# Kernel optimization log

Measured on AMD Instinct MI355X. Metric: run time of the kernel, lower is better.

Reference implementation:

```python
import jax, jax.numpy as jnp
import numpy as np

H = 224; W = 224; ZNEAR = 0.01; ZFAR = 100.0; EPS2D = 0.3
N_GAUSS = 1024; N_CAM = 2
ALPHA_MIN = 1.0 / 255.0; ALPHA_MAX = 0.999


def quat_to_rotmat(q):
    # gsplat convention: wxyz, normalized internally. q: [N,4] -> [N,3,3]
    q = q / jnp.linalg.norm(q, axis=-1, keepdims=True)
    w, x, y, z = q[:, 0], q[:, 1], q[:, 2], q[:, 3]
    R = jnp.stack([
        jnp.stack([1.0 - 2.0 * (y * y + z * z), 2.0 * (x * y - w * z), 2.0 * (x * z + w * y)], -1),
        jnp.stack([2.0 * (x * y + w * z), 1.0 - 2.0 * (x * x + z * z), 2.0 * (y * z - w * x)], -1),
        jnp.stack([2.0 * (x * z - w * y), 2.0 * (y * z + w * x), 1.0 - 2.0 * (x * x + y * y)], -1),
    ], -2)
    return R


def setup_inputs() -> dict:
    key = jax.random.key(0)
    ks = jax.random.split(key, 5)
    xyz = jax.random.normal(ks[0], (N_GAUSS, 3), dtype=jnp.float32) * 0.5
    rgb = jax.random.uniform(ks[1], (N_GAUSS, 3), dtype=jnp.float32)
    opacity = jax.random.uniform(ks[2], (N_GAUSS,), dtype=jnp.float32)
    scale = jax.random.uniform(ks[3], (N_GAUSS, 3), dtype=jnp.float32) * 0.04 + 0.005
    rotation = jax.random.normal(ks[4], (N_GAUSS, 4), dtype=jnp.float32)
    w2c_list = []
    for a in (0.0, 0.3):  # two views, small yaw apart, camera 3 units back
        c, s = np.cos(a), np.sin(a)
        w2c_list.append(np.array([[c, 0, -s, 0], [0, 1, 0, 0], [s, 0, c, 3.0], [0, 0, 0, 1]], dtype=np.float32))
    w2cs = jnp.asarray(np.stack(w2c_list))
    K = np.array([[300.0, 0.0, 112.0], [0.0, 300.0, 112.0], [0.0, 0.0, 1.0]], dtype=np.float32)
    Ks = jnp.asarray(np.stack([K] * N_CAM))
    return {"w2cs": w2cs, "Ks": Ks, "xyz": xyz, "rgb": rgb, "opacity": opacity, "scale": scale, "rotation": rotation}


def _render_one(viewmat, K, means, cov3d, colors, opac, bg):
    R = viewmat[:3, :3]; t = viewmat[:3, 3]
    p_cam = means @ R.T + t                       # [N,3]
    z = p_cam[:, 2]; rz = 1.0 / z
    fx, fy, cx, cy = K[0, 0], K[1, 1], K[0, 2], K[1, 2]
    lim_x = 1.3 * (0.5 * W / fx); lim_y = 1.3 * (0.5 * H / fy)
    tx = z * jnp.clip(p_cam[:, 0] * rz, -lim_x, lim_x)
    ty = z * jnp.clip(p_cam[:, 1] * rz, -lim_y, lim_y)
    # camera-frame 3D covariance, then perspective Jacobian projection to 2D
    cov_cam = jnp.einsum('ij,njk,lk->nil', R, cov3d, R)   # [N,3,3]
    zero = jnp.zeros_like(rz)
    J = jnp.stack([
        jnp.stack([fx * rz, zero, -fx * tx * rz * rz], -1),
        jnp.stack([zero, fy * rz, -fy * ty * rz * rz], -1),
    ], -2)                                                # [N,2,3]
    cov2d = jnp.einsum('nij,njk,nlk->nil', J, cov_cam, J) # [N,2,2]
    a = cov2d[:, 0, 0] + EPS2D; d = cov2d[:, 1, 1] + EPS2D; b = cov2d[:, 0, 1]
    det = a * d - b * b
    ia = d / det; id_ = a / det; ib = -b / det            # inverse of blurred 2D cov
    u = fx * p_cam[:, 0] * rz + cx
    v = fy * p_cam[:, 1] * rz + cy
    valid = (z > ZNEAR) & (z < ZFAR) & (det > 0)
    o = jnp.where(valid, opac, 0.0)
    # front-to-back depth sort (gradients flow through gathered values)
    order = jnp.argsort(z)
    u, v, ia, ib, id_, o = (arr[order] for arr in (u, v, ia, ib, id_, o))
    colors_s = colors[order]
    # pixel centers, row-major flattened grid [P]
    xs = jnp.arange(W, dtype=jnp.float32) + 0.5
    ys = jnp.arange(H, dtype=jnp.float32) + 0.5
    pix_x = jnp.tile(xs, H); pix_y = jnp.repeat(ys, W)
    dx = u[None, :] - pix_x[:, None]                      # [P,N]
    dy = v[None, :] - pix_y[:, None]
    sigma = 0.5 * (ia * dx * dx + id_ * dy * dy) + ib * dx * dy
    alpha = jnp.minimum(o[None, :] * jnp.exp(-sigma), ALPHA_MAX)
    alpha = jnp.where((sigma >= 0.0) & (alpha > ALPHA_MIN), alpha, 0.0)
    log1m = jnp.log1p(-alpha)
    logT = jnp.cumsum(log1m, axis=1)
    T = jnp.exp(logT - log1m)                             # exclusive transmittance
    wgt = alpha * T                                       # [P,N]
    img = wgt @ colors_s                                  # [P,3]
    Tf = jnp.exp(logT[:, -1])
    img = img + Tf[:, None] * bg
    return img.reshape(H, W, 3), (1.0 - Tf).reshape(H, W, 1)


def reference(w2cs, Ks, xyz, rgb, opacity, scale, rotation):
    Rq = quat_to_rotmat(rotation)                         # [N,3,3]
    M = Rq * scale[:, None, :]                            # R @ diag(s)
    cov3d = jnp.einsum('nij,nkj->nik', M, M)              # R S S^T R^T
    bg = jnp.ones((3,), dtype=xyz.dtype)                  # bg_color buffer of ones
    imgs, alphas = jax.vmap(lambda vm, K: _render_one(vm, K, xyz, cov3d, rgb, opacity, bg))(w2cs, Ks)
    return imgs, alphas                                   # rgb [C,H,W,3], mask [C,H,W,1]
```

## Files before the change

kernel.cpp:

```cpp
#include <hip/hip_runtime.h>
#include <math.h>

#define NG 1024
#define NC 2
#define HH 224
#define WW 224
#define TILES_X 28
#define TILES_Y 28
#define EPS2D 0.3f
#define ALPHA_MIN (1.0f/255.0f)
#define ALPHA_MAX 0.999f
#define MAXL 512
#define LOG2E 1.4426950408889634f

__global__ __launch_bounds__(256) void fused_kernel(
        const float* __restrict__ w2cs, const float* __restrict__ Ks,
        const float* __restrict__ xyz, const float* __restrict__ rgb,
        const float* __restrict__ opac, const float* __restrict__ scale,
        const float* __restrict__ rot, float* __restrict__ out) {
    const int cam = blockIdx.z;
    const int TX = blockIdx.x, TY = blockIdx.y;
    const int tid = threadIdx.x;
    const int lane = tid & 63;
    const int wv   = tid >> 6;

    __shared__ union {
        unsigned long long keys[MAXL];
        float4 part[4][64];
    } shu;
    __shared__ float4 sA[MAXL];
    __shared__ float4 sB[MAXL];
    __shared__ float  sC[MAXL];
    __shared__ int    cnt[8];
    __shared__ int    scnt;

    if (tid == 0) scnt = 0;
    __syncthreads();

    const float* vm = w2cs + cam*16;
    const float R00 = vm[0],  R01 = vm[1],  R02 = vm[2],  t0 = vm[3];
    const float R10 = vm[4],  R11 = vm[5],  R12 = vm[6],  t1 = vm[7];
    const float R20 = vm[8],  R21 = vm[9],  R22 = vm[10], t2 = vm[11];
    const float* Kc = Ks + cam*9;
    const float fx = Kc[0], cx = Kc[2], fy = Kc[4], cy = Kc[5];
    const float limx = 1.3f * (0.5f * (float)WW / fx);
    const float limy = 1.3f * (0.5f * (float)HH / fy);

    #pragma unroll
    for (int k = 0; k < 4; k++) {
        int g = k*256 + tid;
        float X = xyz[g*3], Y = xyz[g*3+1], Z = xyz[g*3+2];
        float pz = R20*X + R21*Y + R22*Z + t2;
        float o  = opac[g];
        float tau = __logf(255.f * o);
        bool cand = (pz > 0.01f) && (pz < 100.f) && (tau > 0.f);
        if (cand) {
            float rz = 1.f / pz;
            float px = R00*X + R01*Y + R02*Z + t0;
            float py = R10*X + R11*Y + R12*Z + t1;
            float uu = fx*px*rz + cx;
            float vv = fy*py*rz + cy;
            float sx = scale[g*3+0], sy = scale[g*3+1], sz = scale[g*3+2];
            float smax = fmaxf(sx, fmaxf(sy, sz));
            float j00 = fx*rz, j11 = fy*rz;
            float j02m = fx*limx*rz, j12m = fy*limy*rz;
            float abnd = smax*smax*(j00*j00 + j02m*j02m) + EPS2D;
            float dbnd = smax*smax*(j11*j11 + j12m*j12m) + EPS2D;
            float rx = sqrtf(2.f*tau*abnd) + 0.01f;
            float ry = sqrtf(2.f*tau*dbnd) + 0.01f;
            int xmin = max((int)ceilf (uu - rx - 0.5f), 0);
            int xmax = min((int)floorf(uu + rx - 0.5f), WW-1);
            int ymin = max((int)ceilf (vv - ry - 0.5f), 0);
            int ymax = min((int)floorf(vv + ry - 0.5f), HH-1);
            cand = (xmin <= xmax) && (ymin <= ymax) &&
                   (TX >= (xmin>>3)) && (TX <= (xmax>>3)) &&
                   (TY >= (ymin>>3)) && (TY <= (ymax>>3));
        }
        unsigned long long m = __ballot(cand);
        int cw = __popcll(m);
        if (cw) {
            int basepos = 0;
            if (lane == 0) basepos = atomicAdd(&scnt, cw);
            basepos = __shfl(basepos, 0);
            if (cand) {
                int pos = basepos + __popcll(m & ((1ull << lane) - 1ull));
                if (pos < MAXL)
                    shu.keys[pos] = ((unsigned long long)__float_as_uint(pz) << 10)
                                  | (unsigned long long)g;
            }
        }
    }
    __syncthreads();
    int n = min(scnt, MAXL);

    unsigned long long myk0 = (tid       < n) ? shu.keys[tid]       : 0ull;
    unsigned long long myk1 = (tid + 256 < n) ? shu.keys[tid + 256] : 0ull;
    int r0 = 0, r1 = 0;
    #pragma unroll 4
    for (int j = 0; j < n; j++) {
        unsigned long long kj = shu.keys[j];
        r0 += (kj < myk0) ? 1 : 0;
        r1 += (kj < myk1) ? 1 : 0;
    }
    __syncthreads();
    if (tid       < n) shu.keys[r0] = myk0;
    if (tid + 256 < n) shu.keys[r1] = myk1;
    __syncthreads();

    auto prep = [&](int i, float4 &A, float4 &B, float &C) -> bool {
        if (i >= n) return false;
        int g = (int)(shu.keys[i] & 1023ull);

        float qw = rot[g*4+0], qx = rot[g*4+1], qy = rot[g*4+2], qz = rot[g*4+3];
        float qn = rsqrtf(qw*qw + qx*qx + qy*qy + qz*qz);
        qw *= qn; qx *= qn; qy *= qn; qz *= qn;
        float r00 = 1.f - 2.f*(qy*qy + qz*qz), r01 = 2.f*(qx*qy - qw*qz), r02 = 2.f*(qx*qz + qw*qy);
        float r10 = 2.f*(qx*qy + qw*qz), r11 = 1.f - 2.f*(qx*qx + qz*qz), r12 = 2.f*(qy*qz - qw*qx);
        float r20 = 2.f*(qx*qz - qw*qy), r21 = 2.f*(qy*qz + qw*qx), r22 = 1.f - 2.f*(qx*qx + qy*qy);

        float sx = scale[g*3+0], sy = scale[g*3+1], sz = scale[g*3+2];
        float m00 = r00*sx, m01 = r01*sy, m02 = r02*sz;
        float m10 = r10*sx, m11 = r11*sy, m12 = r12*sz;
        float m20 = r20*sx, m21 = r21*sy, m22 = r22*sz;
        float c00 = m00*m00 + m01*m01 + m02*m02;
        float c01 = m00*m10 + m01*m11 + m02*m12;
        float c02 = m00*m20 + m01*m21 + m02*m22;
        float c11 = m10*m10 + m11*m11 + m12*m12;
        float c12 = m10*m20 + m11*m21 + m12*m22;
        float c22 = m20*m20 + m21*m21 + m22*m22;

        float X = xyz[g*3], Y = xyz[g*3+1], Z = xyz[g*3+2];
        float px = R00*X + R01*Y + R02*Z + t0;
        float py = R10*X + R11*Y + R12*Z + t1;
        float pz = R20*X + R21*Y + R22*Z + t2;
        float rz = 1.f / pz;

        float txc = pz * fminf(fmaxf(px*rz, -limx), limx);
        float tyc = pz * fminf(fmaxf(py*rz, -limy), limy);

        float v00 = R00*c00 + R01*c01 + R02*c02;
        float v01 = R00*c01 + R01*c11 + R02*c12;
        float v02 = R00*c02 + R01*c12 + R02*c22;
        float v10 = R10*c00 + R11*c01 + R12*c02;
        float v11 = R10*c01 + R11*c11 + R12*c12;
        float v12 = R10*c02 + R11*c12 + R12*c22;
        float v20 = R20*c00 + R21*c01 + R22*c02;
        float v21 = R20*c01 + R21*c11 + R22*c12;
        float v22 = R20*c02 + R21*c12 + R22*c22;
        float cc00 = v00*R00 + v01*R01 + v02*R02;
        float cc01 = v00*R10 + v01*R11 + v02*R12;
        float cc02 = v00*R20 + v01*R21 + v02*R22;
        float cc11 = v10*R10 + v11*R11 + v12*R12;
        float cc12 = v10*R20 + v11*R21 + v12*R22;
        float cc22 = v20*R20 + v21*R21 + v22*R22;

        float j00 = fx*rz, j02 = -fx*txc*rz*rz;
        float j11 = fy*rz, j12 = -fy*tyc*rz*rz;
        float a  = j00*j00*cc00 + 2.f*j00*j02*cc02 + j02*j02*cc22 + EPS2D;
        float bq = j00*j11*cc01 + j00*j12*cc02 + j02*j11*cc12 + j02*j12*cc22;
        float d  = j11*j11*cc11 + 2.f*j11*j12*cc12 + j12*j12*cc22 + EPS2D;
        float det = a*d - bq*bq;

        if (!((pz > 0.01f) && (pz < 100.f) && (det > 0.f))) return false;

        float o = opac[g];
        float tau = __logf(255.f * o);
        if (!(tau > 0.f)) return false;

        float hx = sqrtf(2.f*tau*a) + 0.02f;
        float hy = sqrtf(2.f*tau*d) + 0.02f;
        float uu = fx*px*rz + cx;
        float vv = fy*py*rz + cy;
        float xlo = (float)(TX*8) + 0.5f, xhi = (float)(TX*8) + 7.5f;
        float ylo = (float)(TY*8) + 0.5f, yhi = (float)(TY*8) + 7.5f;
        if (uu + hx < xlo || uu - hx > xhi || vv + hy < ylo || vv - hy > yhi)
            return false;

        float idet = 1.f / det;
        A = make_float4(uu, vv, 0.5f*LOG2E*d*idet, -LOG2E*bq*idet);
        B = make_float4(0.5f*LOG2E*a*idet, o, rgb[g*3+0], rgb[g*3+1]);
        C = rgb[g*3+2];
        return true;
    };

    float4 A0, B0, A1, B1; float C0, C1;
    bool kp0 = prep(tid,       A0, B0, C0);
    bool kp1 = prep(tid + 256, A1, B1, C1);

    unsigned long long bal0 = __ballot(kp0);
    unsigned long long bal1 = __ballot(kp1);
    if (lane == 0) { cnt[wv] = __popcll(bal0); cnt[4 + wv] = __popcll(bal1); }
    __syncthreads();
    int base0 = 0, base1 = 0, n2 = 0;
    #pragma unroll
    for (int s = 0; s < 8; s++) {
        int cs = cnt[s];
        base0 += (s < wv)     ? cs : 0;
        base1 += (s < 4 + wv) ? cs : 0;
        n2 += cs;
    }
    unsigned long long lt = (1ull << lane) - 1ull;
    int d0 = base0 + __popcll(bal0 & lt);
    int d1 = base1 + __popcll(bal1 & lt);
    if (kp0) { sA[d0] = A0; sB[d0] = B0; sC[d0] = C0; }
    if (kp1) { sA[d1] = A1; sB[d1] = B1; sC[d1] = C1; }
    __syncthreads();

    const float pxl = (float)(TX*8 + (lane & 7)) + 0.5f;
    const float pyl = (float)(TY*8 + (lane >> 3)) + 0.5f;
    int seglen = (n2 + 3) >> 2;
    int js = wv * seglen;
    int je = min(n2, js + seglen);

    float T = 1.f, cr = 0.f, cg = 0.f, cb = 0.f;
#define CBODY(J) do { \
        float4 ga = sA[J]; float4 gb = sB[J]; float bv = sC[J]; \
        float dx = ga.x - pxl, dy = ga.y - pyl; \
        float sg = ga.z*dx*dx + gb.x*dy*dy + ga.w*dx*dy; \
        float al = fminf(gb.y * exp2f(-sg), ALPHA_MAX); \
        al = (sg >= 0.f && al > ALPHA_MIN) ? al : 0.f; \
        float wgt = al * T; \
        cr += wgt * gb.z; cg += wgt * gb.w; cb += wgt * bv; \
        T -= al * T; \
    } while (0)

    int j = js;
    while (j + 16 <= je) {
        #pragma unroll 4
        for (int q = 0; q < 16; q++) { CBODY(j + q); }
        j += 16;
        if (__all(T < 1e-4f)) break;
    }
    for (; j < je; j++) { CBODY(j); }
#undef CBODY

    shu.part[wv][lane] = make_float4(cr, cg, cb, T);
    __syncthreads();

    if (tid < 64) {
        float4 c0 = shu.part[0][lane];
        float Cr = c0.x, Cg = c0.y, Cb = c0.z, Tp = c0.w;
        #pragma unroll
        for (int s = 1; s < 4; s++) {
            float4 cs = shu.part[s][lane];
            Cr += Tp * cs.x;
            Cg += Tp * cs.y;
            Cb += Tp * cs.z;
            Tp *= cs.w;
        }
        int p = (TY*8 + (lane >> 3)) * WW + TX*8 + (lane & 7);
        float* img = out + (size_t)cam * (HH*WW*3) + (size_t)p * 3;
        img[0] = Cr + Tp;
        img[1] = Cg + Tp;
        img[2] = Cb + Tp;
        out[(size_t)NC*HH*WW*3 + (size_t)cam*(HH*WW) + p] = 1.f - Tp;
    }
}

extern "C" void kernel_launch(void* const* d_in, const int* in_sizes, int n_in,
                              void* d_out, int out_size, void* d_ws, size_t ws_size,
                              hipStream_t stream) {
    const float* w2cs  = (const float*)d_in[0];
    const float* Ks    = (const float*)d_in[1];
    const float* xyz   = (const float*)d_in[2];
    const float* rgb   = (const float*)d_in[3];
    const float* opac  = (const float*)d_in[4];
    const float* scale = (const float*)d_in[5];
    const float* rot   = (const float*)d_in[6];
    float* out = (float*)d_out;

    fused_kernel<<<dim3(TILES_X, TILES_Y, NC), 256, 0, stream>>>(
        w2cs, Ks, xyz, rgb, opac, scale, rot, out);
}
```

Before: 77.94 us.

## Render two 8x8 tiles per block with shared cull/sort and per-tile masks

Each block now covers a 16x8 region (two 8x8 tiles), so the per-block culling, rank sort and Gaussian preparation are amortised over twice as many pixels. Waves are split into two tiles times two depth segments, and a per-Gaussian bitmask lets each wave skip Gaussians that do not touch its tile. The sort keys become doubles compared two at a time, with gaussian ids kept in a separate ushort array, and empty blocks exit early after writing the background. The trade-off is halved grid size and fewer depth segments per pixel, which lengthens the serial compositing chain per wave, and early termination is now checked inside a branchy loop.

After: 80.08 us. 2.7% more time.

```diff
diff --git a/kernel.cpp b/kernel.cpp
--- a/kernel.cpp
+++ b/kernel.cpp
@@ -5,34 +5,37 @@
 #define NC 2
 #define HH 224
 #define WW 224
-#define TILES_X 28
-#define TILES_Y 28
+#define RGX 14
+#define RGY 28
 #define EPS2D 0.3f
 #define ALPHA_MIN (1.0f/255.0f)
 #define ALPHA_MAX 0.999f
 #define MAXL 512
 #define LOG2E 1.4426950408889634f
 
-__global__ __launch_bounds__(256) void fused_kernel(
+__global__ __launch_bounds__(256, 4) void fused_kernel(
         const float* __restrict__ w2cs, const float* __restrict__ Ks,
         const float* __restrict__ xyz, const float* __restrict__ rgb,
         const float* __restrict__ opac, const float* __restrict__ scale,
         const float* __restrict__ rot, float* __restrict__ out) {
     const int cam = blockIdx.z;
-    const int TX = blockIdx.x, TY = blockIdx.y;
+    const int BX = blockIdx.x, TY = blockIdx.y;
     const int tid = threadIdx.x;
     const int lane = tid & 63;
     const int wv   = tid >> 6;
 
     __shared__ union {
-        unsigned long long keys[MAXL];
-        float4 part[4][64];
+        double keys[MAXL];
+        float4 part[2][2][64];
     } shu;
     __shared__ float4 sA[MAXL];
     __shared__ float4 sB[MAXL];
     __shared__ float  sC[MAXL];
-    __shared__ int    cnt[8];
-    __shared__ int    scnt;
+    __shared__ unsigned short gidA[MAXL];
+    __shared__ unsigned short gidS[MAXL];
+    __shared__ unsigned char  mk[MAXL];
+    __shared__ int cnt[8];
+    __shared__ int scnt;
 
     if (tid == 0) scnt = 0;
     __syncthreads();
@@ -45,6 +48,9 @@
     const float fx = Kc[0], cx = Kc[2], fy = Kc[4], cy = Kc[5];
     const float limx = 1.3f * (0.5f * (float)WW / fx);
     const float limy = 1.3f * (0.5f * (float)HH / fy);
+
+    const float xlo = (float)(BX*16) + 0.5f, xhi = (float)(BX*16) + 15.5f;
+    const float ylo = (float)(TY*8)  + 0.5f, yhi = (float)(TY*8)  + 7.5f;
 
     #pragma unroll
     for (int k = 0; k < 4; k++) {
@@ -66,15 +72,10 @@
             float j02m = fx*limx*rz, j12m = fy*limy*rz;
             float abnd = smax*smax*(j00*j00 + j02m*j02m) + EPS2D;
             float dbnd = smax*smax*(j11*j11 + j12m*j12m) + EPS2D;
-            float rx = sqrtf(2.f*tau*abnd) + 0.01f;
-            float ry = sqrtf(2.f*tau*dbnd) + 0.01f;
-            int xmin = max((int)ceilf (uu - rx - 0.5f), 0);
-            int xmax = min((int)floorf(uu + rx - 0.5f), WW-1);
-            int ymin = max((int)ceilf (vv - ry - 0.5f), 0);
-            int ymax = min((int)floorf(vv + ry - 0.5f), HH-1);
-            cand = (xmin <= xmax) && (ymin <= ymax) &&
-                   (TX >= (xmin>>3)) && (TX <= (xmax>>3)) &&
-                   (TY >= (ymin>>3)) && (TY <= (ymax>>3));
+            float rx = sqrtf(2.f*tau*abnd) + 0.03f;
+            float ry = sqrtf(2.f*tau*dbnd) + 0.03f;
+            cand = (uu + rx >= xlo) && (uu - rx <= xhi) &&
+                   (vv + ry >= ylo) && (vv - ry <= yhi);
         }
         unsigned long long m = __ballot(cand);
         int cw = __popcll(m);
@@ -84,32 +85,54 @@
             basepos = __shfl(basepos, 0);
             if (cand) {
                 int pos = basepos + __popcll(m & ((1ull << lane) - 1ull));
-                if (pos < MAXL)
-                    shu.keys[pos] = ((unsigned long long)__float_as_uint(pz) << 10)
-                                  | (unsigned long long)g;
+                if (pos < MAXL) {
+                    float pz2 = R20*X + R21*Y + R22*Z + t2;
+                    shu.keys[pos] = (double)__float_as_uint(pz2) * 1024.0
+                                  + (double)g;
+                    gidA[pos] = (unsigned short)g;
+                }
             }
         }
     }
     __syncthreads();
-    int n = min(scnt, MAXL);
-
-    unsigned long long myk0 = (tid       < n) ? shu.keys[tid]       : 0ull;
-    unsigned long long myk1 = (tid + 256 < n) ? shu.keys[tid + 256] : 0ull;
+    const int n = min(scnt, MAXL);
+
+    if (n == 0) {
+        if (tid < 128) {
+            int ln = tid & 63, lt = tid >> 6;
+            int px = BX*16 + lt*8 + (ln & 7), py = TY*8 + (ln >> 3);
+            int p = py * WW + px;
+            float* img = out + (size_t)cam * (HH*WW*3) + (size_t)p * 3;
+            img[0] = 1.f; img[1] = 1.f; img[2] = 1.f;
+            out[(size_t)NC*HH*WW*3 + (size_t)cam*(HH*WW) + p] = 0.f;
+        }
+        return;
+    }
+
+    const bool h0 = tid < n, h1 = tid + 256 < n;
+    double myk0 = h0 ? shu.keys[tid]       : 0.0;
+    double myk1 = h1 ? shu.keys[tid + 256] : 0.0;
     int r0 = 0, r1 = 0;
-    #pragma unroll 4
-    for (int j = 0; j < n; j++) {
-        unsigned long long kj = shu.keys[j];
-        r0 += (kj < myk0) ? 1 : 0;
-        r1 += (kj < myk1) ? 1 : 0;
-    }
-    __syncthreads();
-    if (tid       < n) shu.keys[r0] = myk0;
-    if (tid + 256 < n) shu.keys[r1] = myk1;
-    __syncthreads();
-
-    auto prep = [&](int i, float4 &A, float4 &B, float &C) -> bool {
+    const int nh = n >> 1;
+    const double2* kp2 = reinterpret_cast<const double2*>(shu.keys);
+    #pragma unroll 2
+    for (int q = 0; q < nh; q++) {
+        double2 kj = kp2[q];
+        r0 += (kj.x < myk0) ? 1 : 0;  r0 += (kj.y < myk0) ? 1 : 0;
+        r1 += (kj.x < myk1) ? 1 : 0;  r1 += (kj.y < myk1) ? 1 : 0;
+    }
+    if (n & 1) {
+        double kj = shu.keys[n-1];
+        r0 += (kj < myk0) ? 1 : 0;  r1 += (kj < myk1) ? 1 : 0;
+    }
+    unsigned short mg0 = h0 ? gidA[tid] : 0, mg1 = h1 ? gidA[tid + 256] : 0;
+    if (h0) gidS[r0] = mg0;
+    if (h1) gidS[r1] = mg1;
+    __syncthreads();
+
+    auto prep = [&](int i, float4 &A, float4 &B, float &C, int &msk) -> bool {
         if (i >= n) return false;
-        int g = (int)(shu.keys[i] & 1023ull);
+        int g = (int)gidS[i];
 
         float qw = rot[g*4+0], qx = rot[g*4+1], qy = rot[g*4+2], qz = rot[g*4+3];
         float qn = rsqrtf(qw*qw + qx*qx + qy*qy + qz*qz);
@@ -171,10 +194,18 @@
         float hy = sqrtf(2.f*tau*d) + 0.02f;
         float uu = fx*px*rz + cx;
         float vv = fy*py*rz + cy;
-        float xlo = (float)(TX*8) + 0.5f, xhi = (float)(TX*8) + 7.5f;
-        float ylo = (float)(TY*8) + 0.5f, yhi = (float)(TY*8) + 7.5f;
-        if (uu + hx < xlo || uu - hx > xhi || vv + hy < ylo || vv - hy > yhi)
-            return false;
+        int xmin = max((int)ceilf (uu - hx - 0.5f), 0);
+        int xmax = min((int)floorf(uu + hx - 0.5f), WW-1);
+        int ymin = max((int)ceilf (vv - hy - 0.5f), 0);
+        int ymax = min((int)floorf(vv + hy - 0.5f), HH-1);
+        if (xmin > xmax || ymin > ymax) return false;
+        int tx0 = xmin >> 3, tx1 = xmax >> 3;
+        int ty0 = ymin >> 3, ty1 = ymax >> 3;
+        if (TY < ty0 || TY > ty1) return false;
+        msk = 0;
+        if (2*BX   >= tx0 && 2*BX   <= tx1) msk |= 1;
+        if (2*BX+1 >= tx0 && 2*BX+1 <= tx1) msk |= 2;
+        if (!msk) return false;
 
         float idet = 1.f / det;
         A = make_float4(uu, vv, 0.5f*LOG2E*d*idet, -LOG2E*bq*idet);
@@ -183,9 +214,9 @@
         return true;
     };
 
-    float4 A0, B0, A1, B1; float C0, C1;
-    bool kp0 = prep(tid,       A0, B0, C0);
-    bool kp1 = prep(tid + 256, A1, B1, C1);
+    float4 A0, B0, A1, B1; float C0 = 0.f, C1 = 0.f; int m0 = 0, m1 = 0;
+    bool kp0 = prep(tid,       A0, B0, C0, m0);
+    bool kp1 = prep(tid + 256, A1, B1, C1, m1);
 
     unsigned long long bal0 = __ballot(kp0);
     unsigned long long bal1 = __ballot(kp1);
@@ -199,56 +230,49 @@
         base1 += (s < 4 + wv) ? cs : 0;
         n2 += cs;
     }
-    unsigned long long lt = (1ull << lane) - 1ull;
-    int d0 = base0 + __popcll(bal0 & lt);
-    int d1 = base1 + __popcll(bal1 & lt);
-    if (kp0) { sA[d0] = A0; sB[d0] = B0; sC[d0] = C0; }
-    if (kp1) { sA[d1] = A1; sB[d1] = B1; sC[d1] = C1; }
-    __syncthreads();
-
-    const float pxl = (float)(TX*8 + (lane & 7)) + 0.5f;
+    const unsigned long long lt64 = (1ull << lane) - 1ull;
+    int d0 = base0 + __popcll(bal0 & lt64);
+    int d1 = base1 + __popcll(bal1 & lt64);
+    if (kp0) { sA[d0] = A0; sB[d0] = B0; sC[d0] = C0; mk[d0] = (unsigned char)m0; }
+    if (kp1) { sA[d1] = A1; sB[d1] = B1; sC[d1] = C1; mk[d1] = (unsigned char)m1; }
+    __syncthreads();
+
+    const int lt = wv & 1, sg = wv >> 1;
+    const float pxl = (float)(BX*16 + lt*8 + (lane & 7)) + 0.5f;
     const float pyl = (float)(TY*8 + (lane >> 3)) + 0.5f;
-    int seglen = (n2 + 3) >> 2;
-    int js = wv * seglen;
+    int seglen = (n2 + 1) >> 1;
+    int js = sg * seglen;
     int je = min(n2, js + seglen);
 
     float T = 1.f, cr = 0.f, cg = 0.f, cb = 0.f;
-#define CBODY(J) do { \
-        float4 ga = sA[J]; float4 gb = sB[J]; float bv = sC[J]; \
-        float dx = ga.x - pxl, dy = ga.y - pyl; \
-        float sg = ga.z*dx*dx + gb.x*dy*dy + ga.w*dx*dy; \
-        float al = fminf(gb.y * exp2f(-sg), ALPHA_MAX); \
-        al = (sg >= 0.f && al > ALPHA_MIN) ? al : 0.f; \
-        float wgt = al * T; \
-        cr += wgt * gb.z; cg += wgt * gb.w; cb += wgt * bv; \
-        T -= al * T; \
-    } while (0)
-
-    int j = js;
-    while (j + 16 <= je) {
-        #pragma unroll 4
-        for (int q = 0; q < 16; q++) { CBODY(j + q); }
-        j += 16;
-        if (__all(T < 1e-4f)) break;
-    }
-    for (; j < je; j++) { CBODY(j); }
-#undef CBODY
-
-    shu.part[wv][lane] = make_float4(cr, cg, cb, T);
-    __syncthreads();
-
-    if (tid < 64) {
-        float4 c0 = shu.part[0][lane];
-        float Cr = c0.x, Cg = c0.y, Cb = c0.z, Tp = c0.w;
-        #pragma unroll
-        for (int s = 1; s < 4; s++) {
-            float4 cs = shu.part[s][lane];
-            Cr += Tp * cs.x;
-            Cg += Tp * cs.y;
-            Cb += Tp * cs.z;
-            Tp *= cs.w;
-        }
-        int p = (TY*8 + (lane >> 3)) * WW + TX*8 + (lane & 7);
+    #pragma unroll 4
+    for (int j = js; j < je; j++) {
+        if ((mk[j] >> lt) & 1) {
+            float4 ga = sA[j]; float4 gb = sB[j]; float bv = sC[j];
+            float dx = ga.x - pxl, dy = ga.y - pyl;
+            float sgm = ga.z*dx*dx + gb.x*dy*dy + ga.w*dx*dy;
+            float al = fminf(gb.y * exp2f(-sgm), ALPHA_MAX);
+            al = (sgm >= 0.f && al > ALPHA_MIN) ? al : 0.f;
+            float wgt = al * T;
+            cr += wgt * gb.z; cg += wgt * gb.w; cb += wgt * bv;
+            T -= al * T;
+        }
+        if (((j - js) & 15) == 15 && __all(T < 1e-4f)) break;
+    }
+
+    shu.part[sg][lt][lane] = make_float4(cr, cg, cb, T);
+    __syncthreads();
+
+    if (tid < 128) {
+        int ln = tid & 63, t2i = tid >> 6;
+        float4 c0 = shu.part[0][t2i][ln];
+        float4 c1 = shu.part[1][t2i][ln];
+        float Cr = c0.x + c0.w * c1.x;
+        float Cg = c0.y + c0.w * c1.y;
+        float Cb = c0.z + c0.w * c1.z;
+        float Tp = c0.w * c1.w;
+        int px = BX*16 + t2i*8 + (ln & 7), py = TY*8 + (ln >> 3);
+        int p = py * WW + px;
         float* img = out + (size_t)cam * (HH*WW*3) + (size_t)p * 3;
         img[0] = Cr + Tp;
         img[1] = Cg + Tp;
@@ -269,6 +293,6 @@
     const float* rot   = (const float*)d_in[6];
     float* out = (float*)d_out;
 
-    fused_kernel<<<dim3(TILES_X, TILES_Y, NC), 256, 0, stream>>>(
+    fused_kernel<<<dim3(RGX, RGY, NC), 256, 0, stream>>>(
         w2cs, Ks, xyz, rgb, opac, scale, rot, out);
 }
```
